# Performance work log

Hardware: AMD Instinct MI355X
Metric: run time of the kernel (lower is better)

Reference implementation:

```python
import jax, jax.numpy as jnp
import numpy as np

B, L, D, H = 2, 2048, 1024, 16
HD = D // H  # head_dim = 64


def setup_inputs() -> dict:
    key = jax.random.key(0)
    ks = jax.random.split(key, 9)
    s = 0.02
    return {
        "x": jax.random.normal(ks[0], (B, L, D), dtype=jnp.float32),
        "wq": jax.random.normal(ks[1], (D, D), dtype=jnp.float32) * s,
        "bq": jnp.zeros((D,), dtype=jnp.float32),
        "wk": jax.random.normal(ks[2], (D, D), dtype=jnp.float32) * s,
        "bk": jnp.zeros((D,), dtype=jnp.float32),
        "wv": jax.random.normal(ks[3], (D, D), dtype=jnp.float32) * s,
        "bv": jnp.zeros((D,), dtype=jnp.float32),
        "wo": jax.random.normal(ks[4], (D, D), dtype=jnp.float32) * s,
        "bo": jnp.zeros((D,), dtype=jnp.float32),
    }


def reference(x, wq, bq, wk, bk, wv, bv, wo, bo):
    b, l, d = x.shape
    # projections -> [B, H, L, HD]
    def split_heads(t):
        return t.reshape(b, l, H, HD).transpose(0, 2, 1, 3)
    q = split_heads(x @ wq + bq)
    k = split_heads(x @ wk + bk)
    v = split_heads(x @ wv + bv)
    scores = jnp.einsum('bhqd,bhkd->bhqk', q, k) / jnp.sqrt(jnp.float32(HD))
    # causal mask via -inf then clamp to [-50, 50]: masked entries become -50 (faithful to torch code)
    mask = jnp.triu(jnp.full((l, l), -jnp.inf, dtype=scores.dtype), k=1)
    scores = jnp.clip(scores + mask[None, None, :, :], -50.0, 50.0)
    attn = jax.nn.softmax(scores, axis=-1)
    # dropout is identity in eval/deterministic mode
    out = jnp.einsum('bhqk,bhkd->bhqd', attn, v)
    out = out.transpose(0, 2, 1, 3).reshape(b, l, d)
    out = out @ wo + bo
    return out, attn
```

## Files before the change

### kernel.cpp

```cpp
#include <hip/hip_runtime.h>
#include <hip/hip_bf16.h>

#define B_  2
#define L_  2048
#define D_  1024
#define H_  16
#define HD_ 64

typedef __bf16 bf16x8 __attribute__((ext_vector_type(8)));
typedef float  f32x4  __attribute__((ext_vector_type(4)));
using bf16_t = __hip_bfloat16;
typedef unsigned int u32;
typedef unsigned long long u64;

static __device__ __forceinline__ f32x4 mfma16(bf16x8 a, bf16x8 b, f32x4 c) {
    return __builtin_amdgcn_mfma_f32_16x16x32_bf16(a, b, c, 0, 0, 0);
}

static __device__ __forceinline__ void gl16(const bf16_t* g, bf16_t* l) {
    __builtin_amdgcn_global_load_lds(
        (const __attribute__((address_space(1))) unsigned int*)g,
        (__attribute__((address_space(3))) unsigned int*)l, 16, 0, 0);
}

static __device__ __forceinline__ u32 cvtpk(float lo, float hi) {
    u32 r;
    asm("v_cvt_pk_bf16_f32 %0, %1, %2" : "=v"(r) : "v"(lo), "v"(hi));
    return r;
}

__global__ __launch_bounds__(256) void k_prep(
        const float* __restrict__ x,
        const float* __restrict__ w0, const float* __restrict__ w1,
        const float* __restrict__ w2, const float* __restrict__ w3,
        bf16_t* __restrict__ xb,
        bf16_t* __restrict__ t0, bf16_t* __restrict__ t1,
        bf16_t* __restrict__ t2, bf16_t* __restrict__ t3) {
    __shared__ bf16_t tile[64][65];
    int z = blockIdx.z;
    int t = threadIdx.x;
    if (z >= 4) {
        int slice = z - 4;
        int lin = blockIdx.y * 16 + blockIdx.x;
        int idx = (slice * 256 + lin) * 256 + t;
        const float4* p = (const float4*)x + (size_t)idx * 2;
        float4 a = p[0], b = p[1];
        union { bf16_t h[8]; bf16x8 v; } u;
        u.h[0] = __float2bfloat16(a.x); u.h[1] = __float2bfloat16(a.y);
        u.h[2] = __float2bfloat16(a.z); u.h[3] = __float2bfloat16(a.w);
        u.h[4] = __float2bfloat16(b.x); u.h[5] = __float2bfloat16(b.y);
        u.h[6] = __float2bfloat16(b.z); u.h[7] = __float2bfloat16(b.w);
        *(bf16x8*)(xb + (size_t)idx * 8) = u.v;
        return;
    }
    const float* w = (z == 0) ? w0 : (z == 1) ? w1 : (z == 2) ? w2 : w3;
    bf16_t* wt     = (z == 0) ? t0 : (z == 1) ? t1 : (z == 2) ? t2 : t3;
    int kb = blockIdx.x * 64, nb = blockIdx.y * 64;
    int r  = t >> 4, c4 = (t & 15) * 4;
    #pragma unroll
    for (int it = 0; it < 4; ++it) {
        int kr = r + it * 16;
        float4 v = *(const float4*)&w[(size_t)(kb + kr) * D_ + nb + c4];
        tile[kr][c4 + 0] = __float2bfloat16(v.x);
        tile[kr][c4 + 1] = __float2bfloat16(v.y);
        tile[kr][c4 + 2] = __float2bfloat16(v.z);
        tile[kr][c4 + 3] = __float2bfloat16(v.w);
    }
    __syncthreads();
    #pragma unroll
    for (int it = 0; it < 4; ++it) {
        int nr = r + it * 16;
        union { bf16_t h[4]; u64 u; } o;
        o.h[0] = tile[c4 + 0][nr];
        o.h[1] = tile[c4 + 1][nr];
        o.h[2] = tile[c4 + 2][nr];
        o.h[3] = tile[c4 + 3][nr];
        *(u64*)&wt[(size_t)(nb + nr) * D_ + kb + c4] = o.u;
    }
}

__global__ __launch_bounds__(256, 3) void k_gemm_qkv(
        const bf16_t* __restrict__ A,
        const bf16_t* __restrict__ Wq, const bf16_t* __restrict__ Wk, const bf16_t* __restrict__ Wv,
        const float* __restrict__ bq, const float* __restrict__ bk, const float* __restrict__ bv,
        bf16_t* __restrict__ Qo, bf16_t* __restrict__ Ko, bf16_t* __restrict__ Vo) {
    __shared__ __align__(16) bf16_t Al[128][32];
    __shared__ __align__(16) bf16_t Bl[128][32];
    const int K = D_;
    int z = blockIdx.z;
    const bf16_t* Wt = (z == 0) ? Wq : (z == 1) ? Wk : Wv;
    const float* bias = (z == 0) ? bq : (z == 1) ? bk : bv;
    bf16_t* outp      = (z == 0) ? Qo : (z == 1) ? Ko : Vo;
    int tid = threadIdx.x, lane = tid & 63, wid = tid >> 6;
    int m0 = blockIdx.y * 128, n0 = blockIdx.x * 128;
    int wm = (wid >> 1) * 64, wn = (wid & 1) * 64;
    int r16 = lane & 15, g = lane >> 4;
    int lrow = lane >> 2, lcol = (lane & 3) * 8;
    f32x4 acc[4][4] = {};
    for (int kb = 0; kb < K; kb += 32) {
        __syncthreads();
        gl16(&A [(size_t)(m0 + wid * 32 + lrow) * K + kb + lcol],      &Al[wid * 32][0]);
        gl16(&A [(size_t)(m0 + wid * 32 + 16 + lrow) * K + kb + lcol], &Al[wid * 32 + 16][0]);
        gl16(&Wt[(size_t)(n0 + wid * 32 + lrow) * K + kb + lcol],      &Bl[wid * 32][0]);
        gl16(&Wt[(size_t)(n0 + wid * 32 + 16 + lrow) * K + kb + lcol], &Bl[wid * 32 + 16][0]);
        __syncthreads();
        bf16x8 af[4], bfr[4];
        #pragma unroll
        for (int i = 0; i < 4; ++i) af[i]  = *(const bf16x8*)&Al[wm + i * 16 + r16][g * 8];
        #pragma unroll
        for (int j = 0; j < 4; ++j) bfr[j] = *(const bf16x8*)&Bl[wn + j * 16 + r16][g * 8];
        #pragma unroll
        for (int i = 0; i < 4; ++i)
            #pragma unroll
            for (int j = 0; j < 4; ++j)
                acc[i][j] = mfma16(af[i], bfr[j], acc[i][j]);
    }
    if (z == 2) {
        #pragma unroll
        for (int i = 0; i < 4; ++i)
            #pragma unroll
            for (int j = 0; j < 4; ++j) {
                int n = n0 + wn + j * 16 + r16;
                float bv2 = bias[n];
                int h = n >> 6, hd = n & 63;
                int m = m0 + wm + i * 16 + g * 4;
                int bb = m >> 11, l0 = m & (L_ - 1);
                u32 lo = cvtpk(acc[i][j][0] + bv2, acc[i][j][1] + bv2);
                u32 hi = cvtpk(acc[i][j][2] + bv2, acc[i][j][3] + bv2);
                u64 pk = ((u64)hi << 32) | lo;
                *(u64*)&Vo[(((size_t)(bb * H_ + h)) * HD_ + hd) * L_ + l0] = pk;
            }
    } else {
        #pragma unroll
        for (int i = 0; i < 4; ++i) {
            #pragma unroll
            for (int j = 0; j < 4; ++j) {
                int n = n0 + wn + j * 16 + r16;
                float bv2 = bias[n];
                int h = n >> 6, hd = n & 63;
                #pragma unroll
                for (int e = 0; e < 4; ++e) {
                    int m = m0 + wm + i * 16 + g * 4 + e;
                    float v = acc[i][j][e] + bv2;
                    int bb = m >> 11, l = m & (L_ - 1);
                    outp[(((size_t)(bb * H_ + h)) * L_ + l) * HD_ + hd] = __float2bfloat16(v);
                }
            }
        }
    }
}

__global__ __launch_bounds__(256, 2) void k_gemm_o(const bf16_t* __restrict__ A,
                                                   const bf16_t* __restrict__ Wt,
                                                   const float* __restrict__ bias,
                                                   float* __restrict__ outp) {
    __shared__ __align__(16) bf16_t Al[128][32];
    __shared__ __align__(16) bf16_t Bl[64][32];
    const int K = D_;
    int tid = threadIdx.x, lane = tid & 63, wid = tid >> 6;
    int m0 = blockIdx.y * 128, n0 = blockIdx.x * 64;
    int wm = (wid >> 1) * 64, wn = (wid & 1) * 32;
    int r16 = lane & 15, g = lane >> 4;
    int lrow = lane >> 2, lcol = (lane & 3) * 8;
    f32x4 acc[4][2] = {};
    for (int kb = 0; kb < K; kb += 32) {
        __syncthreads();
        gl16(&A [(size_t)(m0 + wid * 32 + lrow) * K + kb + lcol],      &Al[wid * 32][0]);
        gl16(&A [(size_t)(m0 + wid * 32 + 16 + lrow) * K + kb + lcol], &Al[wid * 32 + 16][0]);
        gl16(&Wt[(size_t)(n0 + wid * 16 + lrow) * K + kb + lcol],      &Bl[wid * 16][0]);
        __syncthreads();
        bf16x8 af[4], bfr[2];
        #pragma unroll
        for (int i = 0; i < 4; ++i) af[i]  = *(const bf16x8*)&Al[wm + i * 16 + r16][g * 8];
        #pragma unroll
        for (int j = 0; j < 2; ++j) bfr[j] = *(const bf16x8*)&Bl[wn + j * 16 + r16][g * 8];
        #pragma unroll
        for (int i = 0; i < 4; ++i)
            #pragma unroll
            for (int j = 0; j < 2; ++j)
                acc[i][j] = mfma16(af[i], bfr[j], acc[i][j]);
    }
    #pragma unroll
    for (int i = 0; i < 4; ++i)
        #pragma unroll
        for (int j = 0; j < 2; ++j) {
            int n = n0 + wn + j * 16 + r16;
            float bv = bias[n];
            #pragma unroll
            for (int e = 0; e < 4; ++e) {
                int m = m0 + wm + i * 16 + g * 4 + e;
                outp[(size_t)m * D_ + n] = acc[i][j][e] + bv;
            }
        }
}

__global__ __launch_bounds__(256, 4) void k_attn(const bf16_t* __restrict__ Q,
                                                 const bf16_t* __restrict__ Kb,
                                                 const bf16_t* __restrict__ VT,
                                                 bf16_t* __restrict__ ctx,
                                                 float* __restrict__ attn) {
    __shared__ __align__(16) bf16_t K_lds[2][64][64];
    __shared__ __align__(16) bf16_t V_lds[2][64][64];
    int tid = threadIdx.x, lane = tid & 63, wid = tid >> 6;
    int bid = blockIdx.x;
    int r   = bid >> 3;
    int jj  = r & 31, s = r >> 5;
    int bh  = (bid & 7) + 8 * s;
    int j2  = (jj + ((s >> 1) << 4)) & 31;
    int qt  = (s & 1) ? (31 - j2) : j2;
    int b = bh >> 4, h = bh & 15;
    int qb = qt * 64;
    const int diag = qt;
    const bf16_t* Qh = Q  + (size_t)bh * L_ * HD_;
    const bf16_t* Kh = Kb + (size_t)bh * L_ * HD_;
    const bf16_t* Vh = VT + (size_t)bh * HD_ * L_;
    int r16 = lane & 15, g = lane >> 4;
    const float scale2 = 0.125f * 1.44269504088896340736f;
    const float clamp2 = 50.0f * 1.44269504088896340736f;
    int qrow0 = qb + wid * 16;
    int qrow  = qrow0 + r16;

    {
        int zs = qb + 64;
        f32x4 z4 = {0.f, 0.f, 0.f, 0.f};
        for (int rr = 0; rr < 16; ++rr) {
            float* rowp = attn + ((size_t)bh * L_ + qrow0 + rr) * L_;
            for (int c = zs + lane * 4; c < L_; c += 256)
                __builtin_nontemporal_store(z4, (f32x4*)&rowp[c]);
        }
    }

    bf16x8 q0 = *(const bf16x8*)&Qh[(size_t)qrow * HD_ + g * 8];
    bf16x8 q1 = *(const bf16x8*)&Qh[(size_t)qrow * HD_ + 32 + g * 8];

    int srow = lane >> 3, sunit = ((lane & 7) ^ (lane >> 3)) * 8;
    auto STAGE_K = [&](int kt1, int nxt) {
        #pragma unroll
        for (int i = 0; i < 2; ++i) {
            int cb = wid * 16 + i * 8;
            gl16(&Kh[(size_t)(kt1 * 64 + cb + srow) * HD_ + sunit], &K_lds[nxt][cb][0]);
        }
    };
    auto STAGE_V = [&](int kt1, int nxt) {
        #pragma unroll
        for (int i = 0; i < 2; ++i) {
            int cb = wid * 16 + i * 8;
            gl16(&Vh[(size_t)(cb + srow) * L_ + kt1 * 64 + sunit], &V_lds[nxt][cb][0]);
        }
    };

    f32x4 ctxa[4] = {};
    float zsum = 0.f;
    int rx = r16 & 7;

    STAGE_K(0, 0); STAGE_V(0, 0);
    int cur = 0;
    for (int kt = 0; kt <= diag; ++kt) {
        __syncthreads();
        int nxt = cur ^ 1;
        if (kt < diag) { STAGE_K(kt + 1, nxt); STAGE_V(kt + 1, nxt); }
        int kb = kt * 64;
        #pragma unroll
        for (int sub = 0; sub < 2; ++sub) {
            f32x4 sa[2];
            #pragma unroll
            for (int sp = 0; sp < 2; ++sp) {
                int krow = sub * 32 + sp * 16 + r16;
                bf16x8 kf0 = *(const bf16x8*)&K_lds[cur][krow][(g ^ rx) * 8];
                bf16x8 kf1 = *(const bf16x8*)&K_lds[cur][krow][((4 + g) ^ rx) * 8];
                f32x4 zz = {};
                sa[sp] = mfma16(kf1, q1, mfma16(kf0, q0, zz));
            }
            int kb2 = kb + sub * 32;
            u32 dw[2][2];
            #pragma unroll
            for (int sp = 0; sp < 2; ++sp) {
                float ev[4];
                #pragma unroll
                for (int e = 0; e < 4; ++e) {
                    int key = kb2 + sp * 16 + g * 4 + e;
                    float sc = fminf(fmaxf(sa[sp][e] * scale2, -clamp2), clamp2);
                    ev[e] = (key > qrow) ? 0.f : exp2f(sc);
                    zsum += ev[e];
                }
                dw[sp][0] = cvtpk(ev[0], ev[1]);
                dw[sp][1] = cvtpk(ev[2], ev[3]);
            }
            union { u32 u[4]; bf16x8 v; } pa;
            pa.u[0] = dw[0][0]; pa.u[1] = dw[0][1];
            pa.u[2] = dw[1][0]; pa.u[3] = dw[1][1];
            #pragma unroll
            for (int t = 0; t < 4; ++t) {
                int vrow = t * 16 + r16;
                int u0 = ((sub * 4 + (g >> 1)) ^ rx) * 8 + (g & 1) * 4;
                int u1 = ((sub * 4 + 2 + (g >> 1)) ^ rx) * 8 + (g & 1) * 4;
                union { u64 d[2]; bf16x8 v; } vf;
                vf.d[0] = *(const u64*)&V_lds[cur][vrow][u0];
                vf.d[1] = *(const u64*)&V_lds[cur][vrow][u1];
                ctxa[t] = mfma16(pa.v, vf.v, ctxa[t]);
            }
        }
        cur = nxt;
    }

    float v = zsum;
    v += __shfl_xor(v, 16);
    v += __shfl_xor(v, 32);
    float invz = 1.f / v;

    #pragma unroll
    for (int e = 0; e < 4; ++e) {
        float izq = __shfl(invz, g * 4 + e);
        int qr = qrow0 + g * 4 + e;
        #pragma unroll
        for (int t = 0; t < 4; ++t)
            ctx[((size_t)b * L_ + qr) * D_ + h * HD_ + t * 16 + r16] =
                __float2bfloat16(ctxa[t][e] * izq);
    }

    for (int kt = 0; kt <= diag; ++kt) {
        #pragma unroll
        for (int sub = 0; sub < 2; ++sub) {
            int krow0 = kt * 64 + sub * 32;
            #pragma unroll
            for (int sp = 0; sp < 2; ++sp) {
                const bf16_t* kp = &Kh[(size_t)(krow0 + sp * 16 + r16) * HD_ + g * 8];
                bf16x8 kf0 = *(const bf16x8*)kp;
                bf16x8 kf1 = *(const bf16x8*)(kp + 32);
                f32x4 zz = {};
                f32x4 sa = mfma16(kf1, q1, mfma16(kf0, q0, zz));
                int cb = krow0 + sp * 16 + g * 4;
                f32x4 fv;
                #pragma unroll
                for (int e = 0; e < 4; ++e) {
                    int key = cb + e;
                    float sc = fminf(fmaxf(sa[e] * scale2, -clamp2), clamp2);
                    fv[e] = (key > qrow) ? 0.f : exp2f(sc) * invz;
                }
                __builtin_nontemporal_store(fv,
                    (f32x4*)&attn[((size_t)bh * L_ + qrow) * L_ + cb]);
            }
        }
    }
}

extern "C" void kernel_launch(void* const* d_in, const int* in_sizes, int n_in,
                              void* d_out, int out_size, void* d_ws, size_t ws_size,
                              hipStream_t stream) {
    const float* x  = (const float*)d_in[0];
    const float* wq = (const float*)d_in[1];
    const float* bq = (const float*)d_in[2];
    const float* wk = (const float*)d_in[3];
    const float* bk = (const float*)d_in[4];
    const float* wv = (const float*)d_in[5];
    const float* bv = (const float*)d_in[6];
    const float* wo = (const float*)d_in[7];
    const float* bo = (const float*)d_in[8];

    char* ws = (char*)d_ws;
    bf16_t* xb   = (bf16_t*)(ws);
    bf16_t* wqt  = (bf16_t*)(ws + ( 8u << 20));
    bf16_t* wkt  = (bf16_t*)(ws + (10u << 20));
    bf16_t* wvt  = (bf16_t*)(ws + (12u << 20));
    bf16_t* wot  = (bf16_t*)(ws + (14u << 20));
    bf16_t* Qb   = (bf16_t*)(ws + (16u << 20));
    bf16_t* Kbuf = (bf16_t*)(ws + (24u << 20));
    bf16_t* VTb  = (bf16_t*)(ws + (32u << 20));
    bf16_t* ctxb = (bf16_t*)(ws + (40u << 20));

    float* out  = (float*)d_out;
    float* attn = out + (size_t)B_ * L_ * D_;

    dim3 gp(16, 16, 12);
    k_prep<<<gp, 256, 0, stream>>>(x, wq, wk, wv, wo, xb, wqt, wkt, wvt, wot);

    dim3 g3(D_ / 128, (B_ * L_) / 128, 3);
    k_gemm_qkv<<<g3, 256, 0, stream>>>(xb, wqt, wkt, wvt, bq, bk, bv, Qb, Kbuf, VTb);

    k_attn<<<1024, 256, 0, stream>>>(Qb, Kbuf, VTb, ctxb, attn);

    dim3 gg(D_ / 64, (B_ * L_) / 128);
    k_gemm_o<<<gg, 256, 0, stream>>>(ctxb, wot, bo, (float*)d_out);
}
```

Before: 221.8 us.

## Split attention probability writeback into a kernel co-scheduled with output GEMM

The attention kernel now stops after computing the context and stores per-row inverse softmax normalizers to a workspace buffer. A new combined kernel runs the output projection GEMM in its first 512 blocks, and in its remaining blocks it recomputes QK scores and writes the normalized attention probabilities. This lets the write-heavy attn store overlap with the compute-bound output GEMM instead of serializing them. The cost is recomputing the QK^T scores and adding an extra kernel-level split with a small normalizer buffer.

```diff
diff --git a/kernel.cpp b/kernel.cpp
--- a/kernel.cpp
+++ b/kernel.cpp
@@ -150,55 +150,12 @@
     }
 }
 
-__global__ __launch_bounds__(256, 2) void k_gemm_o(const bf16_t* __restrict__ A,
-                                                   const bf16_t* __restrict__ Wt,
-                                                   const float* __restrict__ bias,
-                                                   float* __restrict__ outp) {
-    __shared__ __align__(16) bf16_t Al[128][32];
-    __shared__ __align__(16) bf16_t Bl[64][32];
-    const int K = D_;
-    int tid = threadIdx.x, lane = tid & 63, wid = tid >> 6;
-    int m0 = blockIdx.y * 128, n0 = blockIdx.x * 64;
-    int wm = (wid >> 1) * 64, wn = (wid & 1) * 32;
-    int r16 = lane & 15, g = lane >> 4;
-    int lrow = lane >> 2, lcol = (lane & 3) * 8;
-    f32x4 acc[4][2] = {};
-    for (int kb = 0; kb < K; kb += 32) {
-        __syncthreads();
-        gl16(&A [(size_t)(m0 + wid * 32 + lrow) * K + kb + lcol],      &Al[wid * 32][0]);
-        gl16(&A [(size_t)(m0 + wid * 32 + 16 + lrow) * K + kb + lcol], &Al[wid * 32 + 16][0]);
-        gl16(&Wt[(size_t)(n0 + wid * 16 + lrow) * K + kb + lcol],      &Bl[wid * 16][0]);
-        __syncthreads();
-        bf16x8 af[4], bfr[2];
-        #pragma unroll
-        for (int i = 0; i < 4; ++i) af[i]  = *(const bf16x8*)&Al[wm + i * 16 + r16][g * 8];
-        #pragma unroll
-        for (int j = 0; j < 2; ++j) bfr[j] = *(const bf16x8*)&Bl[wn + j * 16 + r16][g * 8];
-        #pragma unroll
-        for (int i = 0; i < 4; ++i)
-            #pragma unroll
-            for (int j = 0; j < 2; ++j)
-                acc[i][j] = mfma16(af[i], bfr[j], acc[i][j]);
-    }
-    #pragma unroll
-    for (int i = 0; i < 4; ++i)
-        #pragma unroll
-        for (int j = 0; j < 2; ++j) {
-            int n = n0 + wn + j * 16 + r16;
-            float bv = bias[n];
-            #pragma unroll
-            for (int e = 0; e < 4; ++e) {
-                int m = m0 + wm + i * 16 + g * 4 + e;
-                outp[(size_t)m * D_ + n] = acc[i][j][e] + bv;
-            }
-        }
-}
-
-__global__ __launch_bounds__(256, 4) void k_attn(const bf16_t* __restrict__ Q,
-                                                 const bf16_t* __restrict__ Kb,
-                                                 const bf16_t* __restrict__ VT,
-                                                 bf16_t* __restrict__ ctx,
-                                                 float* __restrict__ attn) {
+__global__ __launch_bounds__(256, 4) void k_attn_p1(const bf16_t* __restrict__ Q,
+                                                    const bf16_t* __restrict__ Kb,
+                                                    const bf16_t* __restrict__ VT,
+                                                    bf16_t* __restrict__ ctx,
+                                                    float* __restrict__ attn,
+                                                    float* __restrict__ invzbuf) {
     __shared__ __align__(16) bf16_t K_lds[2][64][64];
     __shared__ __align__(16) bf16_t V_lds[2][64][64];
     int tid = threadIdx.x, lane = tid & 63, wid = tid >> 6;
@@ -307,6 +264,7 @@
     v += __shfl_xor(v, 16);
     v += __shfl_xor(v, 32);
     float invz = 1.f / v;
+    if (g == 0) invzbuf[(size_t)bh * L_ + qrow] = invz;
 
     #pragma unroll
     for (int e = 0; e < 4; ++e) {
@@ -317,6 +275,75 @@
             ctx[((size_t)b * L_ + qr) * D_ + h * HD_ + t * 16 + r16] =
                 __float2bfloat16(ctxa[t][e] * izq);
     }
+}
+
+__global__ __launch_bounds__(256, 4) void k_wr_o(
+        const bf16_t* __restrict__ Q, const bf16_t* __restrict__ Kb,
+        const float* __restrict__ invzbuf, float* __restrict__ attn,
+        const bf16_t* __restrict__ ctxb, const bf16_t* __restrict__ Wo,
+        const float* __restrict__ bo, float* __restrict__ outp) {
+    __shared__ __align__(16) bf16_t Al[128][32];
+    __shared__ __align__(16) bf16_t Bl[64][32];
+    int tid = threadIdx.x, lane = tid & 63, wid = tid >> 6;
+    int bid = blockIdx.x;
+    int r16 = lane & 15, g = lane >> 4;
+
+    if (bid < 512) {
+        const int K = D_;
+        int m0 = (bid >> 4) * 128, n0 = (bid & 15) * 64;
+        int wm = (wid >> 1) * 64, wn = (wid & 1) * 32;
+        int lrow = lane >> 2, lcol = (lane & 3) * 8;
+        f32x4 acc[4][2] = {};
+        for (int kb = 0; kb < K; kb += 32) {
+            __syncthreads();
+            gl16(&ctxb[(size_t)(m0 + wid * 32 + lrow) * K + kb + lcol],      &Al[wid * 32][0]);
+            gl16(&ctxb[(size_t)(m0 + wid * 32 + 16 + lrow) * K + kb + lcol], &Al[wid * 32 + 16][0]);
+            gl16(&Wo  [(size_t)(n0 + wid * 16 + lrow) * K + kb + lcol],      &Bl[wid * 16][0]);
+            __syncthreads();
+            bf16x8 af[4], bfr[2];
+            #pragma unroll
+            for (int i = 0; i < 4; ++i) af[i]  = *(const bf16x8*)&Al[wm + i * 16 + r16][g * 8];
+            #pragma unroll
+            for (int j = 0; j < 2; ++j) bfr[j] = *(const bf16x8*)&Bl[wn + j * 16 + r16][g * 8];
+            #pragma unroll
+            for (int i = 0; i < 4; ++i)
+                #pragma unroll
+                for (int j = 0; j < 2; ++j)
+                    acc[i][j] = mfma16(af[i], bfr[j], acc[i][j]);
+        }
+        #pragma unroll
+        for (int i = 0; i < 4; ++i)
+            #pragma unroll
+            for (int j = 0; j < 2; ++j) {
+                int n = n0 + wn + j * 16 + r16;
+                float bv = bo[n];
+                #pragma unroll
+                for (int e = 0; e < 4; ++e) {
+                    int m = m0 + wm + i * 16 + g * 4 + e;
+                    outp[(size_t)m * D_ + n] = acc[i][j][e] + bv;
+                }
+            }
+        return;
+    }
+
+    int wbid = bid - 512;
+    int r   = wbid >> 3;
+    int jj  = r & 31, s = r >> 5;
+    int bh  = (wbid & 7) + 8 * s;
+    int j2  = (jj + ((s >> 1) << 4)) & 31;
+    int qt  = (s & 1) ? (31 - j2) : j2;
+    int qb = qt * 64;
+    const int diag = qt;
+    const bf16_t* Qh = Q  + (size_t)bh * L_ * HD_;
+    const bf16_t* Kh = Kb + (size_t)bh * L_ * HD_;
+    const float scale2 = 0.125f * 1.44269504088896340736f;
+    const float clamp2 = 50.0f * 1.44269504088896340736f;
+    int qrow0 = qb + wid * 16;
+    int qrow  = qrow0 + r16;
+
+    float invz = invzbuf[(size_t)bh * L_ + qrow];
+    bf16x8 q0 = *(const bf16x8*)&Qh[(size_t)qrow * HD_ + g * 8];
+    bf16x8 q1 = *(const bf16x8*)&Qh[(size_t)qrow * HD_ + 32 + g * 8];
 
     for (int kt = 0; kt <= diag; ++kt) {
         #pragma unroll
@@ -367,6 +394,7 @@
     bf16_t* Kbuf = (bf16_t*)(ws + (24u << 20));
     bf16_t* VTb  = (bf16_t*)(ws + (32u << 20));
     bf16_t* ctxb = (bf16_t*)(ws + (40u << 20));
+    float*  invzbuf = (float*)(ws + (52u << 20));
 
     float* out  = (float*)d_out;
     float* attn = out + (size_t)B_ * L_ * D_;
@@ -377,8 +405,7 @@
     dim3 g3(D_ / 128, (B_ * L_) / 128, 3);
     k_gemm_qkv<<<g3, 256, 0, stream>>>(xb, wqt, wkt, wvt, bq, bk, bv, Qb, Kbuf, VTb);
 
-    k_attn<<<1024, 256, 0, stream>>>(Qb, Kbuf, VTb, ctxb, attn);
-
-    dim3 gg(D_ / 64, (B_ * L_) / 128);
-    k_gemm_o<<<gg, 256, 0, stream>>>(ctxb, wot, bo, (float*)d_out);
-}
+    k_attn_p1<<<1024, 256, 0, stream>>>(Qb, Kbuf, VTb, ctxb, attn, invzbuf);
+
+    k_wr_o<<<1536, 256, 0, stream>>>(Qb, Kbuf, invzbuf, attn, ctxb, wot, bo, out);
+}
```

Measured after the change: 254.0 us. 1.14x slower.
